# Kernel optimization log

Measured on AMD Instinct MI355X. Metric: run time of the kernel, lower is better.

Reference implementation:

```python
import jax, jax.numpy as jnp
import numpy as np

B, T, D_IN, H, D_OUT = 4096, 512, 8, 50, 1

def setup_inputs() -> dict:
    key = jax.random.key(0)
    ks = jax.random.split(key, 7)
    s_ih = 1.0 / np.sqrt(H)
    return {
        "x": jax.random.normal(ks[0], (B, T, D_IN), dtype=jnp.float32),
        # torch nn.RNN params: weight_ih_l0 [H, D_IN], weight_hh_l0 [H, H], biases [H]
        "W_ih": jax.random.uniform(ks[1], (H, D_IN), minval=-s_ih, maxval=s_ih, dtype=jnp.float32),
        "W_hh": jax.random.uniform(ks[2], (H, H), minval=-s_ih, maxval=s_ih, dtype=jnp.float32),
        "b_ih": jax.random.uniform(ks[3], (H,), minval=-s_ih, maxval=s_ih, dtype=jnp.float32),
        "b_hh": jax.random.uniform(ks[4], (H,), minval=-s_ih, maxval=s_ih, dtype=jnp.float32),
        # fc: Linear(H, D_OUT)
        "fc_W": jax.random.uniform(ks[5], (D_OUT, H), minval=-s_ih, maxval=s_ih, dtype=jnp.float32),
        "fc_b": jax.random.uniform(ks[6], (D_OUT,), minval=-s_ih, maxval=s_ih, dtype=jnp.float32),
    }

def reference(x, W_ih, W_hh, b_ih, b_hh, fc_W, fc_b):
    # Vanilla RNN: h_t = tanh(x_t @ W_ih^T + b_ih + h_{t-1} @ W_hh^T + b_hh)
    # Precompute input projections for all timesteps (one big GEMM),
    # then scan the recurrence over time. Only the last hidden state is
    # needed because the module reads out[:, -1, :].
    xW = jnp.einsum('btd,hd->bth', x, W_ih) + (b_ih + b_hh)  # [B, T, H]
    xW_t = jnp.swapaxes(xW, 0, 1)  # [T, B, H] for scan over time

    def step(h, xw_t):
        h_new = jnp.tanh(xw_t + h @ W_hh.T)
        return h_new, None

    h0 = jnp.zeros((x.shape[0], W_hh.shape[0]), dtype=x.dtype)
    h_last, _ = jax.lax.scan(step, h0, xW_t)
    # fc on last timestep hidden
    return h_last @ fc_W.T + fc_b  # [B, D_OUT]
```

## Files before the change

### kernel.cpp

```cpp
#include <hip/hip_runtime.h>

#define B_TOT 4096
#define T_LEN 512
#define DIN   8
#define H_DIM 50

#define ROWS_U 136
#define ROW_UI 68
#define REG_US 2176
#define REG_UI 1088

typedef __attribute__((ext_vector_type(8))) short  short8;
typedef __attribute__((ext_vector_type(4))) float  floatx4;

__device__ __forceinline__ ushort f2bf_rne(float f) {
  uint u = __float_as_uint(f);
  u += 0x7FFFu + ((u >> 16) & 1u);
  return (ushort)(u >> 16);
}
__device__ __forceinline__ ushort f2bf_trunc(float f) {
  return (ushort)(__float_as_uint(f) >> 16);
}
__device__ __forceinline__ float bf2f(ushort b) {
  return __uint_as_float(((uint)b) << 16);
}
__device__ __forceinline__ float fast_tanh(float v) {
  float e = __expf(2.0f * v);
  return 1.0f - 2.0f * __builtin_amdgcn_rcpf(1.0f + e);
}

__global__ __launch_bounds__(256) void rnn_fused(
    const float* __restrict__ x, const float* __restrict__ W_ih,
    const float* __restrict__ W_hh, const float* __restrict__ b_ih,
    const float* __restrict__ b_hh, const float* __restrict__ fc_W,
    const float* __restrict__ fc_b, float* __restrict__ out)
{
  __shared__ __align__(16) ushort lds[2 * REG_US];
  uint* const lds32 = (uint*)lds;

  const int tid  = threadIdx.x;
  const int lane = tid & 63;
  const int wave = tid >> 6;
  const int col  = lane & 15;
  const int kg   = lane >> 4;
  const int b0   = blockIdx.x * 16;

  const int nG = wave * 16 + col;
  const bool live = (nG < H_DIM);
  union U8 { ushort u[8]; short8 v; };
  short8 Bs[4], Bw[4];
#pragma unroll
  for (int c = 0; c < 4; ++c) {
    U8 bs, bw;
#pragma unroll
    for (int j2 = 0; j2 < 4; ++j2) {
      const int p = c * 16 + kg * 4 + j2;
      float w = 0.f;
      if (live) {
        if (p < H_DIM)            w = W_hh[nG * H_DIM + p];
        else if (p < H_DIM + DIN) w = W_ih[nG * DIN + (p - H_DIM)];
      }
      ushort hi = f2bf_rne(w);
      ushort lo = f2bf_trunc(w - bf2f(hi));
      bs.u[2 * j2]     = hi;  bs.u[2 * j2 + 1] = lo;
      bw.u[2 * j2]     = lo;  bw.u[2 * j2 + 1] = hi;
    }
    Bs[c] = bs.v;
    Bw[c] = bw.v;
  }
  const float bv = live ? (b_ih[nG] + b_hh[nG]) : 0.f;
  const floatx4 biasf = {bv, bv, bv, bv};
  const floatx4 zf    = {0.f, 0.f, 0.f, 0.f};

  for (int z = tid; z < 2 * REG_UI; z += 256) lds32[z] = 0;
  __syncthreads();

  const int xm = tid >> 3;
  const int xd = tid & 7;
  const bool xthr = (tid < 128);
  const float* xp = x + ((size_t)(b0 + (xthr ? xm : 0)) * T_LEN) * DIN + xd;
  float px1 = 0.f, px2 = 0.f, px3 = 0.f;
  if (xthr) {
    float x0 = xp[0];
    ushort hi = f2bf_rne(x0);
    ushort lo = f2bf_trunc(x0 - bf2f(hi));
    lds32[xm * ROW_UI + H_DIM + xd] = (uint)hi | ((uint)lo << 16);
    px1 = xp[8]; px2 = xp[16]; px3 = xp[24];
  }
  __syncthreads();

  auto step = [&](int t, const ushort* lp, uint* q32) {
    const int rb = col * ROWS_U + kg * 8;
    short8 A0 = *(const short8*)(lp + rb);
    short8 A1 = *(const short8*)(lp + rb + 32);
    short8 A2 = *(const short8*)(lp + rb + 64);
    short8 A3 = *(const short8*)(lp + rb + 96);

    floatx4 ch0 = biasf;
    ch0 = __builtin_amdgcn_mfma_f32_16x16x32_bf16(A0, Bs[0], ch0, 0, 0, 0);
    ch0 = __builtin_amdgcn_mfma_f32_16x16x32_bf16(A1, Bs[1], ch0, 0, 0, 0);
    floatx4 ch1 = zf;
    ch1 = __builtin_amdgcn_mfma_f32_16x16x32_bf16(A0, Bw[0], ch1, 0, 0, 0);
    ch1 = __builtin_amdgcn_mfma_f32_16x16x32_bf16(A1, Bw[1], ch1, 0, 0, 0);
    floatx4 ch2 = zf;
    ch2 = __builtin_amdgcn_mfma_f32_16x16x32_bf16(A2, Bs[2], ch2, 0, 0, 0);
    ch2 = __builtin_amdgcn_mfma_f32_16x16x32_bf16(A3, Bs[3], ch2, 0, 0, 0);
    floatx4 ch3 = zf;
    ch3 = __builtin_amdgcn_mfma_f32_16x16x32_bf16(A2, Bw[2], ch3, 0, 0, 0);
    ch3 = __builtin_amdgcn_mfma_f32_16x16x32_bf16(A3, Bw[3], ch3, 0, 0, 0);
    floatx4 vsum = (ch0 + ch1) + (ch2 + ch3);

    if (live) {
#pragma unroll
      for (int r = 0; r < 4; ++r) {
        float th = fast_tanh(vsum[r]);
        ushort hi = f2bf_rne(th);
        ushort lo = f2bf_trunc(th - bf2f(hi));
        q32[(kg * 4 + r) * ROW_UI + nG] = (uint)hi | ((uint)lo << 16);
      }
    }
    if (xthr) {
      ushort hi = f2bf_rne(px1);
      ushort lo = f2bf_trunc(px1 - bf2f(hi));
      q32[xm * ROW_UI + H_DIM + xd] = (uint)hi | ((uint)lo << 16);
      px1 = px2; px2 = px3;
      int tn = t + 4; if (tn > T_LEN - 1) tn = T_LEN - 1;
      px3 = xp[(size_t)tn * DIN];
    }
    __syncthreads();
  };

  for (int t = 0; t < T_LEN; t += 2) {
    step(t,     lds,          lds32 + REG_UI);
    step(t + 1, lds + REG_US, lds32);
  }

  if (tid < 64) {
    int m = lane >> 2, kq = lane & 3;
    float accr = 0.f;
    for (int k = kq; k < H_DIM; k += 4) {
      uint pk = lds32[m * ROW_UI + k];
      float hv = bf2f((ushort)(pk & 0xFFFFu)) + bf2f((ushort)(pk >> 16));
      accr += hv * fc_W[k];
    }
    accr += __shfl_xor(accr, 1);
    accr += __shfl_xor(accr, 2);
    if (kq == 0) out[b0 + m] = accr + fc_b[0];
  }
}

extern "C" void kernel_launch(void* const* d_in, const int* in_sizes, int n_in,
                              void* d_out, int out_size, void* d_ws, size_t ws_size,
                              hipStream_t stream) {
  const float* x    = (const float*)d_in[0];
  const float* W_ih = (const float*)d_in[1];
  const float* W_hh = (const float*)d_in[2];
  const float* b_ih = (const float*)d_in[3];
  const float* b_hh = (const float*)d_in[4];
  const float* fc_W = (const float*)d_in[5];
  const float* fc_b = (const float*)d_in[6];
  rnn_fused<<<dim3(B_TOT / 16), dim3(256), 0, stream>>>(
      x, W_ih, W_hh, b_ih, b_hh, fc_W, fc_b, (float*)d_out);
}
```

Baseline: 321.3 us.

## Process two 16-row batch tiles per block to interleave independent MFMA chains

Each block now handles 32 batch rows as two independent 16-row tiles. Every timestep issues two independent sets of MFMAs, interleaved across accumulators, which is meant to hide MFMA and LDS latency on the serial recurrence and spread one barrier over twice the work. The grid halves to 128 blocks, so fewer CUs are used on a 256-CU part. Occupancy is hinted at one block per CU through launch bounds.

```diff
diff --git a/kernel.cpp b/kernel.cpp
--- a/kernel.cpp
+++ b/kernel.cpp
@@ -29,13 +29,13 @@
   return 1.0f - 2.0f * __builtin_amdgcn_rcpf(1.0f + e);
 }
 
-__global__ __launch_bounds__(256) void rnn_fused(
+__global__ __launch_bounds__(256, 1) void rnn_fused(
     const float* __restrict__ x, const float* __restrict__ W_ih,
     const float* __restrict__ W_hh, const float* __restrict__ b_ih,
     const float* __restrict__ b_hh, const float* __restrict__ fc_W,
     const float* __restrict__ fc_b, float* __restrict__ out)
 {
-  __shared__ __align__(16) ushort lds[2 * REG_US];
+  __shared__ __align__(16) ushort lds[4 * REG_US];
   uint* const lds32 = (uint*)lds;
 
   const int tid  = threadIdx.x;
@@ -43,7 +43,7 @@
   const int wave = tid >> 6;
   const int col  = lane & 15;
   const int kg   = lane >> 4;
-  const int b0   = blockIdx.x * 16;
+  const int b0   = blockIdx.x * 32;
 
   const int nG = wave * 16 + col;
   const bool live = (nG < H_DIM);
@@ -72,57 +72,77 @@
   const floatx4 biasf = {bv, bv, bv, bv};
   const floatx4 zf    = {0.f, 0.f, 0.f, 0.f};
 
-  for (int z = tid; z < 2 * REG_UI; z += 256) lds32[z] = 0;
+  for (int z = tid; z < 4 * REG_UI; z += 256) lds32[z] = 0;
   __syncthreads();
 
-  const int xm = tid >> 3;
-  const int xd = tid & 7;
-  const bool xthr = (tid < 128);
-  const float* xp = x + ((size_t)(b0 + (xthr ? xm : 0)) * T_LEN) * DIN + xd;
-  float px1 = 0.f, px2 = 0.f, px3 = 0.f;
-  if (xthr) {
+  const int xrow = tid >> 3;
+  const int xd   = tid & 7;
+  const int xoff = (xrow < 16 ? 0 * REG_UI + xrow * ROW_UI
+                              : 2 * REG_UI + (xrow - 16) * ROW_UI) + H_DIM + xd;
+  const float* xp = x + ((size_t)(b0 + xrow) * T_LEN) * DIN + xd;
+  float px1, px2, px3;
+  {
     float x0 = xp[0];
     ushort hi = f2bf_rne(x0);
     ushort lo = f2bf_trunc(x0 - bf2f(hi));
-    lds32[xm * ROW_UI + H_DIM + xd] = (uint)hi | ((uint)lo << 16);
+    lds32[xoff] = (uint)hi | ((uint)lo << 16);
     px1 = xp[8]; px2 = xp[16]; px3 = xp[24];
   }
   __syncthreads();
 
-  auto step = [&](int t, const ushort* lp, uint* q32) {
+  auto step = [&](int t, int pUS, int qUI) {
     const int rb = col * ROWS_U + kg * 8;
-    short8 A0 = *(const short8*)(lp + rb);
-    short8 A1 = *(const short8*)(lp + rb + 32);
-    short8 A2 = *(const short8*)(lp + rb + 64);
-    short8 A3 = *(const short8*)(lp + rb + 96);
+    const ushort* lpA = lds + pUS + rb;
+    const ushort* lpB = lds + pUS + 2 * REG_US + rb;
+    short8 A0 = *(const short8*)(lpA);
+    short8 A1 = *(const short8*)(lpA + 32);
+    short8 A2 = *(const short8*)(lpA + 64);
+    short8 A3 = *(const short8*)(lpA + 96);
+    short8 B0 = *(const short8*)(lpB);
+    short8 B1 = *(const short8*)(lpB + 32);
+    short8 B2 = *(const short8*)(lpB + 64);
+    short8 B3 = *(const short8*)(lpB + 96);
 
-    floatx4 ch0 = biasf;
-    ch0 = __builtin_amdgcn_mfma_f32_16x16x32_bf16(A0, Bs[0], ch0, 0, 0, 0);
-    ch0 = __builtin_amdgcn_mfma_f32_16x16x32_bf16(A1, Bs[1], ch0, 0, 0, 0);
-    floatx4 ch1 = zf;
-    ch1 = __builtin_amdgcn_mfma_f32_16x16x32_bf16(A0, Bw[0], ch1, 0, 0, 0);
-    ch1 = __builtin_amdgcn_mfma_f32_16x16x32_bf16(A1, Bw[1], ch1, 0, 0, 0);
-    floatx4 ch2 = zf;
-    ch2 = __builtin_amdgcn_mfma_f32_16x16x32_bf16(A2, Bs[2], ch2, 0, 0, 0);
-    ch2 = __builtin_amdgcn_mfma_f32_16x16x32_bf16(A3, Bs[3], ch2, 0, 0, 0);
-    floatx4 ch3 = zf;
-    ch3 = __builtin_amdgcn_mfma_f32_16x16x32_bf16(A2, Bw[2], ch3, 0, 0, 0);
-    ch3 = __builtin_amdgcn_mfma_f32_16x16x32_bf16(A3, Bw[3], ch3, 0, 0, 0);
-    floatx4 vsum = (ch0 + ch1) + (ch2 + ch3);
+    floatx4 a0 = biasf, a1 = zf, a2 = zf, a3 = zf;
+    a0 = __builtin_amdgcn_mfma_f32_16x16x32_bf16(A0, Bs[0], a0, 0, 0, 0);
+    a1 = __builtin_amdgcn_mfma_f32_16x16x32_bf16(A0, Bw[0], a1, 0, 0, 0);
+    a2 = __builtin_amdgcn_mfma_f32_16x16x32_bf16(A2, Bs[2], a2, 0, 0, 0);
+    a3 = __builtin_amdgcn_mfma_f32_16x16x32_bf16(A2, Bw[2], a3, 0, 0, 0);
+    a0 = __builtin_amdgcn_mfma_f32_16x16x32_bf16(A1, Bs[1], a0, 0, 0, 0);
+    a1 = __builtin_amdgcn_mfma_f32_16x16x32_bf16(A1, Bw[1], a1, 0, 0, 0);
+    a2 = __builtin_amdgcn_mfma_f32_16x16x32_bf16(A3, Bs[3], a2, 0, 0, 0);
+    a3 = __builtin_amdgcn_mfma_f32_16x16x32_bf16(A3, Bw[3], a3, 0, 0, 0);
+    floatx4 c0 = biasf, c1 = zf, c2 = zf, c3 = zf;
+    c0 = __builtin_amdgcn_mfma_f32_16x16x32_bf16(B0, Bs[0], c0, 0, 0, 0);
+    c1 = __builtin_amdgcn_mfma_f32_16x16x32_bf16(B0, Bw[0], c1, 0, 0, 0);
+    c2 = __builtin_amdgcn_mfma_f32_16x16x32_bf16(B2, Bs[2], c2, 0, 0, 0);
+    c3 = __builtin_amdgcn_mfma_f32_16x16x32_bf16(B2, Bw[2], c3, 0, 0, 0);
+    c0 = __builtin_amdgcn_mfma_f32_16x16x32_bf16(B1, Bs[1], c0, 0, 0, 0);
+    c1 = __builtin_amdgcn_mfma_f32_16x16x32_bf16(B1, Bw[1], c1, 0, 0, 0);
+    c2 = __builtin_amdgcn_mfma_f32_16x16x32_bf16(B3, Bs[3], c2, 0, 0, 0);
+    c3 = __builtin_amdgcn_mfma_f32_16x16x32_bf16(B3, Bw[3], c3, 0, 0, 0);
+
+    floatx4 vA = (a0 + a1) + (a2 + a3);
+    floatx4 vB = (c0 + c1) + (c2 + c3);
 
     if (live) {
+      uint* qA = lds32 + qUI;
+      uint* qB = lds32 + qUI + 2 * REG_UI;
 #pragma unroll
       for (int r = 0; r < 4; ++r) {
-        float th = fast_tanh(vsum[r]);
-        ushort hi = f2bf_rne(th);
-        ushort lo = f2bf_trunc(th - bf2f(hi));
-        q32[(kg * 4 + r) * ROW_UI + nG] = (uint)hi | ((uint)lo << 16);
+        float thA = fast_tanh(vA[r]);
+        float thB = fast_tanh(vB[r]);
+        ushort hA = f2bf_rne(thA), lA = f2bf_trunc(thA - bf2f(hA));
+        ushort hB = f2bf_rne(thB), lB = f2bf_trunc(thB - bf2f(hB));
+        const int row = (kg * 4 + r) * ROW_UI + nG;
+        qA[row] = (uint)hA | ((uint)lA << 16);
+        qB[row] = (uint)hB | ((uint)lB << 16);
       }
     }
-    if (xthr) {
+    {
       ushort hi = f2bf_rne(px1);
       ushort lo = f2bf_trunc(px1 - bf2f(hi));
-      q32[xm * ROW_UI + H_DIM + xd] = (uint)hi | ((uint)lo << 16);
+      lds32[qUI + xoff] = (uint)hi | ((uint)lo << 16);
       px1 = px2; px2 = px3;
       int tn = t + 4; if (tn > T_LEN - 1) tn = T_LEN - 1;
       px3 = xp[(size_t)tn * DIN];
@@ -131,15 +151,17 @@
   };
 
   for (int t = 0; t < T_LEN; t += 2) {
-    step(t,     lds,          lds32 + REG_UI);
-    step(t + 1, lds + REG_US, lds32);
+    step(t,     0,      REG_UI);
+    step(t + 1, REG_US, 0);
   }
 
-  if (tid < 64) {
-    int m = lane >> 2, kq = lane & 3;
+  if (tid < 128) {
+    int m = tid >> 2, kq = tid & 3;
+    const uint* hrow = lds32 + (m < 16 ? m * ROW_UI
+                                       : 2 * REG_UI + (m - 16) * ROW_UI);
     float accr = 0.f;
     for (int k = kq; k < H_DIM; k += 4) {
-      uint pk = lds32[m * ROW_UI + k];
+      uint pk = hrow[k];
       float hv = bf2f((ushort)(pk & 0xFFFFu)) + bf2f((ushort)(pk >> 16));
       accr += hv * fc_W[k];
     }
@@ -159,6 +181,6 @@
   const float* b_hh = (const float*)d_in[4];
   const float* fc_W = (const float*)d_in[5];
   const float* fc_b = (const float*)d_in[6];
-  rnn_fused<<<dim3(B_TOT / 16), dim3(256), 0, stream>>>(
+  rnn_fused<<<dim3(B_TOT / 32), dim3(256), 0, stream>>>(
       x, W_ih, W_hh, b_ih, b_hh, fc_W, fc_b, (float*)d_out);
 }
```

Result: slower. 383.2 us (+19.3%).
